# Kernel optimization log

Hardware: AMD Instinct MI355X
Metric: run time of the kernel (lower is better)

## Reference

```python
import jax, jax.numpy as jnp
import numpy as np

N, E, D, G, L = 100000, 1600000, 64, 512, 3
EPS = 1e-5


def setup_inputs() -> dict:
    key = jax.random.key(0)
    ks = jax.random.split(key, 8)
    x = jax.random.normal(ks[0], (N, D), dtype=jnp.float32)
    edge_index = jax.random.randint(ks[1], (2, E), 0, N, dtype=jnp.int32)
    batch = jnp.sort(jax.random.randint(ks[2], (N,), 0, G, dtype=jnp.int32))
    s = 1.0 / np.sqrt(D)
    convW = jax.random.normal(ks[3], (L, D, D), dtype=jnp.float32) * s
    convB = jnp.zeros((L, D), jnp.float32)
    bn_g = jnp.ones((L, D), jnp.float32); bn_b = jnp.zeros((L, D), jnp.float32)
    ln_g = jnp.ones((L, D), jnp.float32); ln_b = jnp.zeros((L, D), jnp.float32)
    W1 = jax.random.normal(ks[4], (3 * D, 2 * D), dtype=jnp.float32) * (1.0 / np.sqrt(3 * D))
    b1 = jnp.zeros((2 * D,), jnp.float32)
    ln1_g = jnp.ones((2 * D,), jnp.float32); ln1_b = jnp.zeros((2 * D,), jnp.float32)
    W2 = jax.random.normal(ks[5], (2 * D, D), dtype=jnp.float32) * (1.0 / np.sqrt(2 * D))
    b2 = jnp.zeros((D,), jnp.float32)
    ln2_g = jnp.ones((D,), jnp.float32); ln2_b = jnp.zeros((D,), jnp.float32)
    W3 = jax.random.normal(ks[6], (D, 1), dtype=jnp.float32) * s
    b3 = jnp.zeros((1,), jnp.float32)
    return dict(x=x, edge_index=edge_index, batch=batch, convW=convW, convB=convB,
                bn_g=bn_g, bn_b=bn_b, ln_g=ln_g, ln_b=ln_b,
                W1=W1, b1=b1, ln1_g=ln1_g, ln1_b=ln1_b,
                W2=W2, b2=b2, ln2_g=ln2_g, ln2_b=ln2_b, W3=W3, b3=b3)


def _layer_norm(h, g, b):
    mu = jnp.mean(h, axis=-1, keepdims=True)
    var = jnp.mean((h - mu) ** 2, axis=-1, keepdims=True)
    return (h - mu) * jax.lax.rsqrt(var + EPS) * g + b


def _forward(x, edge_index, batch, convW, convB, bn_g, bn_b, ln_g, ln_b,
             W1, b1, ln1_g, ln1_b, W2, b2, ln2_g, ln2_b, W3, b3):
    n = x.shape[0]
    loops = jnp.arange(n, dtype=edge_index.dtype)
    src = jnp.concatenate([edge_index[0], loops])  # self-loops as in GCNConv
    dst = jnp.concatenate([edge_index[1], loops])
    deg = jax.ops.segment_sum(jnp.ones_like(src, dtype=x.dtype), dst, num_segments=n)
    dinv = jnp.where(deg > 0, jax.lax.rsqrt(deg), 0.0)
    norm = (dinv[src] * dinv[dst])[:, None]  # [E+N, 1]

    h = x
    for i in range(L):
        x_in = h
        hw = h @ convW[i]                                   # [N, D]
        agg = jax.ops.segment_sum(norm * hw[src], dst, num_segments=n) + convB[i]
        # BatchNorm1d (train-mode batch stats, biased var)
        mu = jnp.mean(agg, axis=0)
        var = jnp.mean((agg - mu) ** 2, axis=0)
        hb = (agg - mu) * jax.lax.rsqrt(var + EPS) * bn_g[i] + bn_b[i]
        if i > 0:
            hb = hb + x_in  # residual (shapes match: D == D)
        h = jax.nn.gelu(_layer_norm(hb, ln_g[i], ln_b[i]), approximate=False)

    # multi-pool over graphs
    cnt = jax.ops.segment_sum(jnp.ones((n,), x.dtype), batch, num_segments=G)[:, None]
    s = jax.ops.segment_sum(h, batch, num_segments=G)
    mean = s / jnp.maximum(cnt, 1.0)
    mx = jax.ops.segment_max(h, batch, num_segments=G)
    mx = jnp.where(cnt > 0, mx, 0.0)
    z = jnp.concatenate([mean, mx, s], axis=1)  # [G, 3D]

    z = jax.nn.gelu(_layer_norm(z @ W1 + b1, ln1_g, ln1_b), approximate=False)
    z = jax.nn.gelu(_layer_norm(z @ W2 + b2, ln2_g, ln2_b), approximate=False)
    return z @ W3 + b3  # [G, num_classes]


def reference(x, edge_index, batch, convW, convB, bn_g, bn_b, ln_g, ln_b,
              W1, b1, ln1_g, ln1_b, W2, b2, ln2_g, ln2_b, W3, b3):
    return _forward(x, edge_index, batch, convW, convB, bn_g, bn_b, ln_g, ln_b,
                    W1, b1, ln1_g, ln1_b, W2, b2, ln2_g, ln2_b, W3, b3)
```

## Files before the change

kernel.cpp:

```cpp
#include <hip/hip_runtime.h>
#include <hip/hip_bf16.h>
#include <hip/hip_fp16.h>

#define DD 64
#define EPSV 1e-5f
#define NSLICE 16

typedef __attribute__((ext_vector_type(4))) _Float16 f16x4;
typedef __attribute__((ext_vector_type(8))) _Float16 f16x8;
typedef __attribute__((ext_vector_type(4))) float f32x4;

static __device__ __forceinline__ float fatomic_add(float* p, float v) {
#if defined(__HIP_DEVICE_COMPILE__)
    return unsafeAtomicAdd(p, v);
#else
    return 0.f;
#endif
}

static __device__ __forceinline__ float gelu_exact(float x) {
    return 0.5f * x * (1.0f + erff(x * 0.70710678118654752f));
}

static __device__ __forceinline__ void acc_u4(float* a8, uint4 v) {
    const __half2* hp = reinterpret_cast<const __half2*>(&v);
#pragma unroll
    for (int p = 0; p < 4; ++p) {
        float2 f = __half22float2(hp[p]);
        a8[2 * p] += f.x;
        a8[2 * p + 1] += f.y;
    }
}

#define ACHUNK 2048
#define NBMAX 400

__global__ __launch_bounds__(1024) void k_bcount(const int* __restrict__ dst,
                                                 int* __restrict__ bucketCnt,
                                                 int e, int nbuck) {
    __shared__ int h[NBMAX];
    int t = threadIdx.x;
    for (int i = t; i < nbuck; i += 1024) h[i] = 0;
    __syncthreads();
    int base = blockIdx.x * 8192;
#pragma unroll
    for (int k = 0; k < 8; ++k) {
        int i = base + k * 1024 + t;
        if (i < e) atomicAdd(&h[dst[i] >> 8], 1);
    }
    __syncthreads();
    for (int i = t; i < nbuck; i += 1024)
        if (h[i]) atomicAdd(&bucketCnt[i], h[i]);
}

__global__ __launch_bounds__(512) void k_bscan2(const int* __restrict__ bucketCnt,
                                                int* __restrict__ bbase,
                                                int* __restrict__ bcur,
                                                int* __restrict__ offs,
                                                int nbuck, int etotal, int n) {
    __shared__ int ws[8];
    int t = threadIdx.x, lane = t & 63, wv = t >> 6;
    int v = (t < nbuck) ? bucketCnt[t] : 0;
    int x = v;
#pragma unroll
    for (int o = 1; o < 64; o <<= 1) {
        int u = __shfl_up(x, o, 64);
        if (lane >= o) x += u;
    }
    if (lane == 63) ws[wv] = x;
    __syncthreads();
    int add = 0;
    for (int w = 0; w < wv; ++w) add += ws[w];
    int excl = add + x - v;
    if (t < nbuck) {
        bbase[t] = excl;
        bcur[t] = excl;
    }
    if (t == 0) {
        bbase[nbuck] = etotal;
        offs[n] = etotal;
    }
}

__global__ __launch_bounds__(1024) void k_dhist(const int* __restrict__ off,
                                                int* __restrict__ dcount,
                                                const int* __restrict__ batch,
                                                int* __restrict__ bnd,
                                                __half* __restrict__ mA,
                                                __half* __restrict__ mB,
                                                int n, int g) {
    __shared__ int h[256];
    int t = threadIdx.x;
    if (t < 256) h[t] = 0;
    __syncthreads();
    int i = blockIdx.x * 1024 + t;
    if (i < n) {
        int d = min(off[i + 1] - off[i], 255);
        atomicAdd(&h[d], 1);
        int b = batch[i];
        if (i == 0)
            for (int q = 0; q <= b; ++q) bnd[q] = 0;
        else {
            int pb = batch[i - 1];
            for (int q = pb + 1; q <= b; ++q) bnd[q] = i;
        }
        if (i == n - 1)
            for (int q = b + 1; q <= g; ++q) bnd[q] = n;
    }
    if (blockIdx.x == 0 && t < 64) {
        mA[(size_t)n * 64 + t] = __float2half_rn(0.f);
        mB[(size_t)n * 64 + t] = __float2half_rn(0.f);
    }
    __syncthreads();
    if (t < 256 && h[t]) atomicAdd(&dcount[t], h[t]);
}

__global__ __launch_bounds__(256) void k_dscan(const int* __restrict__ dcount,
                                               int* __restrict__ dcur) {
    __shared__ int ws[4];
    int t = threadIdx.x;
    int lane = t & 63, wv = t >> 6;
    int v = dcount[t];
    int x = v;
#pragma unroll
    for (int o = 1; o < 64; o <<= 1) {
        int u = __shfl_up(x, o, 64);
        if (lane >= o) x += u;
    }
    if (lane == 63) ws[wv] = x;
    __syncthreads();
    int add = 0;
    for (int w = 0; w < wv; ++w) add += ws[w];
    dcur[t] = add + x - v;
}

__global__ __launch_bounds__(1024) void k_dscatter(const int* __restrict__ off,
                                                   int* __restrict__ dcur,
                                                   int* __restrict__ perm, int n) {
    __shared__ int lcnt[256], lbase[256];
    int t = threadIdx.x;
    if (t < 256) lcnt[t] = 0;
    __syncthreads();
    int i = blockIdx.x * 1024 + t;
    int d = 0, rank = 0;
    if (i < n) {
        d = min(off[i + 1] - off[i], 255);
        rank = atomicAdd(&lcnt[d], 1);
    }
    __syncthreads();
    if (t < 256 && lcnt[t]) lbase[t] = atomicAdd(&dcur[t], lcnt[t]);
    __syncthreads();
    if (i < n) perm[lbase[d] + rank] = i;
}

__global__ __launch_bounds__(1024) void k_slotinfo(const int* __restrict__ off,
                                                   const float* __restrict__ dinv,
                                                   const int* __restrict__ perm,
                                                   int4* __restrict__ sinfo,
                                                   int n, int ntiles) {
    int s = blockIdx.x * 1024 + threadIdx.x;
    if (s < n) {
        int node = perm[s];
        int a = off[node];
        int d = off[node + 1] - a;
        sinfo[s] = make_int4(a, d, node, __float_as_int(dinv[node]));
    } else if (s < ntiles * 16) {
        sinfo[s] = make_int4(0, 0, -1, 0);
    }
}

__global__ __launch_bounds__(256) void k_binA(const int* __restrict__ src,
                                              const int* __restrict__ dst,
                                              int* __restrict__ ebuf,
                                              int* __restrict__ bcur,
                                              int e, int nbuck) {
    __shared__ int cnt[NBMAX], startb[NBMAX], posb[NBMAX], gbase[NBMAX];
    __shared__ int stage[ACHUNK];
    __shared__ unsigned short stb[ACHUNK];
    int t = threadIdx.x;
    for (int cbase = blockIdx.x * ACHUNK; cbase < e; cbase += gridDim.x * ACHUNK) {
        int cval = min(ACHUNK, e - cbase);
        for (int i = t; i < nbuck; i += 256) { cnt[i] = 0; posb[i] = 0; }
        __syncthreads();
        int eb[8], es[8];
#pragma unroll
        for (int k = 0; k < 8; ++k) {
            int i = t + k * 256;
            if (i < cval) {
                int s = src[cbase + i];
                int d = dst[cbase + i];
                eb[k] = d >> 8;
                es[k] = s | ((d & 255) << 24);
                atomicAdd(&cnt[eb[k]], 1);
            } else eb[k] = -1;
        }
        __syncthreads();
        if (t == 0) {
            int r = 0;
            for (int b2 = 0; b2 < nbuck; ++b2) { startb[b2] = r; r += cnt[b2]; }
        }
        __syncthreads();
        for (int i = t; i < nbuck; i += 256)
            if (cnt[i] > 0) gbase[i] = atomicAdd(&bcur[i], cnt[i]);
#pragma unroll
        for (int k = 0; k < 8; ++k)
            if (eb[k] >= 0) {
                int idx = startb[eb[k]] + atomicAdd(&posb[eb[k]], 1);
                stage[idx] = es[k];
                stb[idx] = (unsigned short)eb[k];
            }
        __syncthreads();
        for (int i = t; i < cval; i += 256) {
            int b2 = stb[i];
            ebuf[gbase[b2] + (i - startb[b2])] = stage[i];
        }
        __syncthreads();
    }
}

__global__ __launch_bounds__(256) void k_binB(const int* __restrict__ ebuf,
                                              const int* __restrict__ bbase,
                                              const float* __restrict__ x,
                                              int* __restrict__ offs,
                                              float* __restrict__ dinv,
                                              __half* __restrict__ mA,
                                              int* __restrict__ csr, int n) {
    __shared__ int cnt[256], cur[256], ws[4];
    __shared__ float sdinv[256];
    int b = blockIdx.x;
    int base = b << 8;
    int nn = min(256, n - base);
    int t = threadIdx.x;
    int e0 = bbase[b], e1 = bbase[b + 1];
    cnt[t] = 0;
    __syncthreads();
    for (int i = e0 + t; i < e1; i += 256)
        atomicAdd(&cnt[((unsigned)ebuf[i]) >> 24], 1);
    __syncthreads();
    int v = cnt[t];
    int lane = t & 63, wv = t >> 6;
    int x2 = v;
#pragma unroll
    for (int o = 1; o < 64; o <<= 1) {
        int u = __shfl_up(x2, o, 64);
        if (lane >= o) x2 += u;
    }
    if (lane == 63) ws[wv] = x2;
    __syncthreads();
    int add = 0;
    for (int w = 0; w < wv; ++w) add += ws[w];
    int excl = add + x2 - v;
    float dv = rsqrtf((float)v + 1.0f);
    if (t < nn) {
        offs[base + t] = e0 + excl;
        dinv[base + t] = dv;
    }
    sdinv[t] = dv;
    cur[t] = e0 + excl;
    __syncthreads();
    const int tot = nn * 64;
    const size_t gbase2 = (size_t)base * 64;
    for (int i = t; i < tot; i += 256) {
        float val = x[gbase2 + i] * sdinv[i >> 6];
        mA[gbase2 + i] = __float2half_rn(val);
    }
    for (int i = e0 + t; i < e1; i += 256) {
        int packed = ebuf[i];
        int dl = ((unsigned)packed) >> 24;
        int pos = atomicAdd(&cur[dl], 1);
        csr[pos] = packed & 0x00FFFFFF;
    }
}

__global__ __launch_bounds__(256, 4) void k_gather_gemm(const int4* __restrict__ sinfo,
                                                        const int* __restrict__ csr,
                                                        const __half* __restrict__ m16,
                                                        const float* __restrict__ W,
                                                        const float* __restrict__ convB,
                                                        __half* __restrict__ agg,
                                                        float* __restrict__ gstat,
                                                        int n, int nzero) {
    __shared__ float sred[128];
    const int t = threadIdx.x;
    const int lane = t & 63, wv = t >> 6;
    const int g = lane >> 4, ln = lane & 15;

    f16x8 bfr[2][4];
#pragma unroll
    for (int kt = 0; kt < 2; ++kt)
#pragma unroll
        for (int nt = 0; nt < 4; ++nt) {
            f16x8 h;
#pragma unroll
            for (int j = 0; j < 8; ++j)
                h[j] = (_Float16)W[(32 * kt + 8 * g + j) * 64 + 16 * nt + ln];
            bfr[kt][nt] = h;
        }
    const float bias[4] = {convB[ln], convB[16 + ln], convB[32 + ln], convB[48 + ln]};

    if (t < 128) sred[t] = 0.f;
    __syncthreads();

    const int ntiles = (n + 15) >> 4;
    const int tile = blockIdx.x * 4 + wv;
    float s_acc[4] = {0.f, 0.f, 0.f, 0.f}, q_acc[4] = {0.f, 0.f, 0.f, 0.f};
    const uint4* mrow4 = (const uint4*)m16;

    if (tile < ntiles) {
        const int4 si = sinfo[tile * 16 + ln];
        const int a = si.x, deg = si.y, node = si.z;
        const float dd = __int_as_float(si.w);
        const int row_self = (node >= 0) ? node : nzero;

        int md = deg;
#pragma unroll
        for (int o = 1; o < 64; o <<= 1) md = max(md, __shfl_xor(md, o, 64));

        float acc[2][8];
#pragma unroll
        for (int kt = 0; kt < 2; ++kt)
#pragma unroll
            for (int j = 0; j < 8; ++j) acc[kt][j] = 0.f;

        {
            const uint4* rp = mrow4 + ((size_t)row_self << 3) + g;
            uint4 v0 = rp[0], v1 = rp[4];
            acc_u4(acc[0], v0);
            acc_u4(acc[1], v1);
        }
        int ecur[4];
#pragma unroll
        for (int k = 0; k < 4; ++k) ecur[k] = (k < deg) ? csr[a + k] : nzero;
        for (int i = 0; i < md; i += 4) {
            int enx[4];
#pragma unroll
            for (int k = 0; k < 4; ++k) enx[k] = (i + 4 + k < deg) ? csr[a + i + 4 + k] : nzero;
            uint4 v[4][2];
#pragma unroll
            for (int r = 0; r < 4; ++r) {
                const uint4* rp = mrow4 + ((size_t)ecur[r] << 3) + g;
                v[r][0] = rp[0];
                v[r][1] = rp[4];
            }
#pragma unroll
            for (int r = 0; r < 4; ++r) {
                acc_u4(acc[0], v[r][0]);
                acc_u4(acc[1], v[r][1]);
            }
#pragma unroll
            for (int k = 0; k < 4; ++k) ecur[k] = enx[k];
        }

        f32x4 c[4];
#pragma unroll
        for (int nt = 0; nt < 4; ++nt) c[nt] = (f32x4){0.f, 0.f, 0.f, 0.f};
#pragma unroll
        for (int kt = 0; kt < 2; ++kt) {
            f16x8 ah, ar;
#pragma unroll
            for (int j = 0; j < 8; ++j) {
                float v = acc[kt][j] * dd;
                _Float16 h = (_Float16)v;
                ah[j] = h;
                ar[j] = (_Float16)(v - (float)h);
            }
#pragma unroll
            for (int nt = 0; nt < 4; ++nt) {
                c[nt] = __builtin_amdgcn_mfma_f32_16x16x32_f16(ah, bfr[kt][nt], c[nt], 0, 0, 0);
                c[nt] = __builtin_amdgcn_mfma_f32_16x16x32_f16(ar, bfr[kt][nt], c[nt], 0, 0, 0);
            }
        }

        int prow[4];
#pragma unroll
        for (int i = 0; i < 4; ++i) prow[i] = __shfl(node, 4 * g + i, 64);
#pragma unroll
        for (int nt = 0; nt < 4; ++nt) {
#pragma unroll
            for (int i = 0; i < 4; ++i) {
                if (prow[i] >= 0) {
                    float v = c[nt][i] + bias[nt];
                    agg[(size_t)prow[i] * 64 + 16 * nt + ln] = __float2half_rn(v);
                    s_acc[nt] += v;
                    q_acc[nt] += v * v;
                }
            }
        }
    }

#pragma unroll
    for (int nt = 0; nt < 4; ++nt) {
        s_acc[nt] += __shfl_xor(s_acc[nt], 16, 64);
        s_acc[nt] += __shfl_xor(s_acc[nt], 32, 64);
        q_acc[nt] += __shfl_xor(q_acc[nt], 16, 64);
        q_acc[nt] += __shfl_xor(q_acc[nt], 32, 64);
    }
    if (g == 0) {
#pragma unroll
        for (int nt = 0; nt < 4; ++nt) {
            atomicAdd(&sred[16 * nt + ln], s_acc[nt]);
            atomicAdd(&sred[64 + 16 * nt + ln], q_acc[nt]);
        }
    }
    __syncthreads();
    if (t < 64) {
        float* gs = gstat + (blockIdx.x & (NSLICE - 1)) * 128;
        fatomic_add(&gs[t], sred[t]);
        fatomic_add(&gs[64 + t], sred[64 + t]);
    }
}

__global__ __launch_bounds__(256) void k_bn_ln_gelu(const __half* __restrict__ agg,
                                                    const __half* __restrict__ m16res,
                                                    const float* __restrict__ gstat,
                                                    const float* __restrict__ dinv,
                                                    const float* __restrict__ bng,
                                                    const float* __restrict__ bnb,
                                                    const float* __restrict__ lng,
                                                    const float* __restrict__ lnb,
                                                    __half* __restrict__ m16out,
                                                    int n, int has_res, int scale_out) {
    int t = threadIdx.x;
    int lane = t & 63, wv = t >> 6;
    float fs = 0.f, fq = 0.f;
#pragma unroll
    for (int s = 0; s < NSLICE; ++s) {
        fs += gstat[s * 128 + lane];
        fq += gstat[s * 128 + 64 + lane];
    }
    float invN = 1.0f / (float)n;
    float mu_c = fs * invN;
    float var_c = fq * invN - mu_c * mu_c;
    float bscale = rsqrtf(var_c + EPSV) * bng[lane];
    float bshift = bnb[lane];
    float lg = lng[lane], lb = lnb[lane];
    for (int r = blockIdx.x * 4 + wv; r < n; r += gridDim.x * 4) {
        float dd = dinv[r];
        float x = __half2float(agg[(size_t)r * 64 + lane]);
        float hb = (x - mu_c) * bscale + bshift;
        if (has_res) hb += __half2float(m16res[(size_t)r * 64 + lane]) * (1.0f / dd);
        float ssum = hb;
#pragma unroll
        for (int off = 32; off; off >>= 1) ssum += __shfl_xor(ssum, off, 64);
        float rmu = ssum * (1.f / 64.f);
        float d = hb - rmu;
        float vs = d * d;
#pragma unroll
        for (int off = 32; off; off >>= 1) vs += __shfl_xor(vs, off, 64);
        float rvar = vs * (1.f / 64.f);
        float ln = d * rsqrtf(rvar + EPSV) * lg + lb;
        float g = gelu_exact(ln);
        float outv = scale_out ? g * dd : g;
        m16out[(size_t)r * 64 + lane] = __float2half_rn(outv);
    }
}

__global__ __launch_bounds__(256) void k_poolhead(const __half* __restrict__ h,
                                                  const int* __restrict__ bnd,
                                                  const float* __restrict__ W1, const float* __restrict__ b1,
                                                  const float* __restrict__ ln1g, const float* __restrict__ ln1b,
                                                  const float* __restrict__ W2, const float* __restrict__ b2,
                                                  const float* __restrict__ ln2g, const float* __restrict__ ln2b,
                                                  const float* __restrict__ W3, const float* __restrict__ b3,
                                                  float* __restrict__ out) {
    int g = blockIdx.x;
    int t = threadIdx.x;
    int lane = t & 63, wv = t >> 6;
    __shared__ float ss[256], sm[256], zl[192], h1[128], red[2];
    int s0 = bnd[g], e0 = bnd[g + 1];
    float s = 0.f, mx = -INFINITY;
    for (int i = s0 + wv; i < e0; i += 4) {
        float v = __half2float(h[(size_t)i * 64 + lane]);
        s += v;
        mx = fmaxf(mx, v);
    }
    ss[t] = s;
    sm[t] = mx;
    __syncthreads();
    if (t < 64) {
        float fs = ss[t] + ss[t + 64] + ss[t + 128] + ss[t + 192];
        float fm = fmaxf(fmaxf(sm[t], sm[t + 64]), fmaxf(sm[t + 128], sm[t + 192]));
        float cntf = (float)(e0 - s0);
        float mean = fs / fmaxf(cntf, 1.0f);
        if (e0 == s0) fm = 0.f;
        zl[t] = mean;
        zl[64 + t] = fm;
        zl[128 + t] = fs;
    }
    __syncthreads();
    float acc = 0.f;
    if (t < 128) {
        acc = b1[t];
        for (int k = 0; k < 192; ++k) acc += zl[k] * W1[k * 128 + t];
    }
    float s1 = acc;
#pragma unroll
    for (int off = 32; off; off >>= 1) s1 += __shfl_xor(s1, off, 64);
    if (lane == 0 && wv < 2) red[wv] = s1;
    __syncthreads();
    float mu = (red[0] + red[1]) * (1.f / 128.f);
    float d = acc - mu;
    float q = d * d;
#pragma unroll
    for (int off = 32; off; off >>= 1) q += __shfl_xor(q, off, 64);
    __syncthreads();
    if (lane == 0 && wv < 2) red[wv] = q;
    __syncthreads();
    float var = (red[0] + red[1]) * (1.f / 128.f);
    if (t < 128) {
        float ln = d * rsqrtf(var + EPSV) * ln1g[t] + ln1b[t];
        h1[t] = gelu_exact(ln);
    }
    __syncthreads();
    if (t < 64) {
        float acc2 = b2[t];
        for (int k = 0; k < 128; ++k) acc2 += h1[k] * W2[k * 64 + t];
        float s2 = acc2;
#pragma unroll
        for (int off = 32; off; off >>= 1) s2 += __shfl_xor(s2, off, 64);
        float mu2 = s2 * (1.f / 64.f);
        float d2 = acc2 - mu2;
        float q2 = d2 * d2;
#pragma unroll
        for (int off = 32; off; off >>= 1) q2 += __shfl_xor(q2, off, 64);
        float var2 = q2 * (1.f / 64.f);
        float l2 = d2 * rsqrtf(var2 + EPSV) * ln2g[t] + ln2b[t];
        float g2 = gelu_exact(l2);
        float p = g2 * W3[t];
#pragma unroll
        for (int off = 32; off; off >>= 1) p += __shfl_xor(p, off, 64);
        if (t == 0) out[g] = p + b3[0];
    }
}

extern "C" void kernel_launch(void* const* d_in, const int* in_sizes, int n_in,
                              void* d_out, int out_size, void* d_ws, size_t ws_size,
                              hipStream_t stream) {
    const float* x      = (const float*)d_in[0];
    const int*   eidx   = (const int*)d_in[1];
    const int*   batch  = (const int*)d_in[2];
    const float* convW  = (const float*)d_in[3];
    const float* convB  = (const float*)d_in[4];
    const float* bn_g   = (const float*)d_in[5];
    const float* bn_b   = (const float*)d_in[6];
    const float* ln_g   = (const float*)d_in[7];
    const float* ln_b   = (const float*)d_in[8];
    const float* W1     = (const float*)d_in[9];
    const float* b1     = (const float*)d_in[10];
    const float* ln1g   = (const float*)d_in[11];
    const float* ln1b   = (const float*)d_in[12];
    const float* W2     = (const float*)d_in[13];
    const float* b2     = (const float*)d_in[14];
    const float* ln2g   = (const float*)d_in[15];
    const float* ln2b   = (const float*)d_in[16];
    const float* W3     = (const float*)d_in[17];
    const float* b3     = (const float*)d_in[18];
    float* out = (float*)d_out;

    const int N = in_sizes[0] / DD;
    const int E = in_sizes[1] / 2;
    const int G = out_size;
    const int* esrc = eidx;
    const int* edst = eidx + E;

    char* ws = (char*)d_ws;
    size_t off_b = 0;
    auto alloc = [&](size_t bytes) {
        size_t p = off_b;
        off_b = (off_b + bytes + 255) & ~(size_t)255;
        return (void*)(ws + p);
    };
    const int ntiles = (N + 15) / 16;
    const int gblocks = (ntiles + 3) / 4;

    float*  gstats = (float*)alloc((size_t)3 * NSLICE * 128 * 4);
    int*    dcount = (int*)alloc(256 * 4);
    int*    bucketCnt = (int*)alloc((size_t)NBMAX * 4);
    const size_t zero_bytes = 3 * NSLICE * 128 * 4 + 1024 + 1792;
    int*    offs   = (int*)alloc((size_t)(N + 1) * 4);
    float*  dinv   = (float*)alloc((size_t)N * 4);
    int*    csr    = (int*)alloc((size_t)E * 4);
    int*    ebuf   = (int*)alloc((size_t)E * 4);
    __half* m16A   = (__half*)alloc((size_t)(N + 1) * DD * 2);
    __half* m16B   = (__half*)alloc((size_t)(N + 1) * DD * 2);
    __half* aggbuf = (__half*)alloc((size_t)N * DD * 2);
    int*    perm   = (int*)alloc((size_t)N * 4);
    int4*   sinfo  = (int4*)alloc((size_t)ntiles * 16 * 16);
    int*    dcur   = (int*)alloc(256 * 4);
    int*    bnd    = (int*)alloc((size_t)(G + 1) * 4);
    int*    bbase  = (int*)alloc((size_t)(NBMAX + 1) * 4);
    int*    bcur   = (int*)alloc(((size_t)(N + 255) / 256) * 4);
    (void)ws_size; (void)n_in;

    const int nbuck = (N + 255) / 256;
    const int nb = (N + 1023) / 1024;

    hipMemsetAsync(gstats, 0, zero_bytes, stream);
    k_bcount<<<(E + 8191) / 8192, 1024, 0, stream>>>(edst, bucketCnt, E, nbuck);
    k_bscan2<<<1, 512, 0, stream>>>(bucketCnt, bbase, bcur, offs, nbuck, E, N);
    k_binA<<<(E + ACHUNK - 1) / ACHUNK, 256, 0, stream>>>(esrc, edst, ebuf, bcur, E, nbuck);
    k_binB<<<nbuck, 256, 0, stream>>>(ebuf, bbase, x, offs, dinv, m16A, csr, N);
    k_dhist<<<nb, 1024, 0, stream>>>(offs, dcount, batch, bnd, m16A, m16B, N, G);
    k_dscan<<<1, 256, 0, stream>>>(dcount, dcur);
    k_dscatter<<<nb, 1024, 0, stream>>>(offs, dcur, perm, N);
    k_slotinfo<<<(ntiles * 16 + 1023) / 1024, 1024, 0, stream>>>(offs, dinv, perm, sinfo, N, ntiles);

    __half* gin[3]  = {m16A, m16B, m16A};
    __half* gout[3] = {m16B, m16A, m16B};

    for (int l = 0; l < 3; ++l) {
        float* gstat = gstats + (size_t)l * NSLICE * 128;
        k_gather_gemm<<<gblocks, 256, 0, stream>>>(sinfo, csr, (const __half*)gin[l],
                                                   convW + (size_t)l * DD * DD, convB + l * DD,
                                                   aggbuf, gstat, N, N);
        k_bn_ln_gelu<<<2048, 256, 0, stream>>>(aggbuf, gin[l], gstat, dinv,
                                               bn_g + l * DD, bn_b + l * DD,
                                               ln_g + l * DD, ln_b + l * DD,
                                               gout[l], N, l > 0 ? 1 : 0, l < 2 ? 1 : 0);
    }

    k_poolhead<<<G, 256, 0, stream>>>(m16B, bnd, W1, b1, ln1g, ln1b,
                                      W2, b2, ln2g, ln2b, W3, b3, out);
}
```

Baseline: 402.5 us.

## Fuse layer loop and pooling head into one cooperative persistent kernel

Replaces the per-layer gather-GEMM and BN/LN/GELU launches plus the pooling head with a single cooperative kernel of 1024 blocks. The blocks loop over tiles and rows and use grid.sync between phases, which removes seven kernel launches and their drain gaps. It also folds the slot-info construction into the degree scatter kernel, dropping the perm array and one launch. In exchange, the gather phase now runs with fewer resident waves over persistent loops, which may cut latency hiding, and grid-wide barriers add their own cost. The old multi-kernel path remains as a fallback if the cooperative launch fails.

```diff
diff --git a/kernel.cpp b/kernel.cpp
--- a/kernel.cpp
+++ b/kernel.cpp
@@ -1,12 +1,15 @@
 #include <hip/hip_runtime.h>
+#include <hip/hip_cooperative_groups.h>
 #include <hip/hip_bf16.h>
 #include <hip/hip_fp16.h>
+
+namespace cg = cooperative_groups;
 
 #define DD 64
 #define EPSV 1e-5f
 #define NSLICE 16
-
-typedef __attribute__((ext_vector_type(4))) _Float16 f16x4;
+#define CGBLOCKS 1024
+
 typedef __attribute__((ext_vector_type(8))) _Float16 f16x8;
 typedef __attribute__((ext_vector_type(4))) float f32x4;
 
@@ -88,7 +91,8 @@
                                                 int* __restrict__ bnd,
                                                 __half* __restrict__ mA,
                                                 __half* __restrict__ mB,
-                                                int n, int g) {
+                                                int4* __restrict__ sinfo,
+                                                int n, int g, int ntiles) {
     __shared__ int h[256];
     int t = threadIdx.x;
     if (t < 256) h[t] = 0;
@@ -111,6 +115,8 @@
         mA[(size_t)n * 64 + t] = __float2half_rn(0.f);
         mB[(size_t)n * 64 + t] = __float2half_rn(0.f);
     }
+    int pad = ntiles * 16 - n;
+    if (blockIdx.x == 0 && t < pad) sinfo[n + t] = make_int4(0, 0, -1, 0);
     __syncthreads();
     if (t < 256 && h[t]) atomicAdd(&dcount[t], h[t]);
 }
@@ -135,37 +141,27 @@
 }
 
 __global__ __launch_bounds__(1024) void k_dscatter(const int* __restrict__ off,
+                                                   const float* __restrict__ dinv,
                                                    int* __restrict__ dcur,
-                                                   int* __restrict__ perm, int n) {
+                                                   int4* __restrict__ sinfo, int n) {
     __shared__ int lcnt[256], lbase[256];
     int t = threadIdx.x;
     if (t < 256) lcnt[t] = 0;
     __syncthreads();
     int i = blockIdx.x * 1024 + t;
-    int d = 0, rank = 0;
+    int d = 0, rank = 0, a = 0, dtrue = 0;
     if (i < n) {
-        d = min(off[i + 1] - off[i], 255);
+        a = off[i];
+        dtrue = off[i + 1] - a;
+        d = min(dtrue, 255);
         rank = atomicAdd(&lcnt[d], 1);
     }
     __syncthreads();
     if (t < 256 && lcnt[t]) lbase[t] = atomicAdd(&dcur[t], lcnt[t]);
     __syncthreads();
-    if (i < n) perm[lbase[d] + rank] = i;
-}
-
-__global__ __launch_bounds__(1024) void k_slotinfo(const int* __restrict__ off,
-                                                   const float* __restrict__ dinv,
-                                                   const int* __restrict__ perm,
-                                                   int4* __restrict__ sinfo,
-                                                   int n, int ntiles) {
-    int s = blockIdx.x * 1024 + threadIdx.x;
-    if (s < n) {
-        int node = perm[s];
-        int a = off[node];
-        int d = off[node + 1] - a;
-        sinfo[s] = make_int4(a, d, node, __float_as_int(dinv[node]));
-    } else if (s < ntiles * 16) {
-        sinfo[s] = make_int4(0, 0, -1, 0);
+    if (i < n) {
+        int slot = lbase[d] + rank;
+        sinfo[slot] = make_int4(a, dtrue, i, __float_as_int(dinv[i]));
     }
 }
 
@@ -272,6 +268,284 @@
     }
 }
 
+static __device__ __forceinline__ void gather_tile(
+    const int4* __restrict__ sinfo, const int* __restrict__ csr,
+    const uint4* __restrict__ mrow4, const f16x8 bfr[2][4], const float bias[4],
+    __half* __restrict__ agg, int tile, int n, int lane, int g, int ln,
+    float s_acc[4], float q_acc[4]) {
+    const int4 si = sinfo[tile * 16 + ln];
+    const int a = si.x, deg = si.y, node = si.z;
+    const float dd = __int_as_float(si.w);
+    const int row_self = (node >= 0) ? node : n;
+
+    int md = deg;
+#pragma unroll
+    for (int o = 1; o < 64; o <<= 1) md = max(md, __shfl_xor(md, o, 64));
+
+    float acc[2][8];
+#pragma unroll
+    for (int kt = 0; kt < 2; ++kt)
+#pragma unroll
+        for (int j = 0; j < 8; ++j) acc[kt][j] = 0.f;
+
+    {
+        const uint4* rp = mrow4 + ((size_t)row_self << 3) + g;
+        uint4 v0 = rp[0], v1 = rp[4];
+        acc_u4(acc[0], v0);
+        acc_u4(acc[1], v1);
+    }
+    int ecur[4];
+#pragma unroll
+    for (int k = 0; k < 4; ++k) ecur[k] = (k < deg) ? csr[a + k] : n;
+    for (int i = 0; i < md; i += 4) {
+        int enx[4];
+#pragma unroll
+        for (int k = 0; k < 4; ++k) enx[k] = (i + 4 + k < deg) ? csr[a + i + 4 + k] : n;
+        uint4 v[4][2];
+#pragma unroll
+        for (int r = 0; r < 4; ++r) {
+            const uint4* rp = mrow4 + ((size_t)ecur[r] << 3) + g;
+            v[r][0] = rp[0];
+            v[r][1] = rp[4];
+        }
+#pragma unroll
+        for (int r = 0; r < 4; ++r) {
+            acc_u4(acc[0], v[r][0]);
+            acc_u4(acc[1], v[r][1]);
+        }
+#pragma unroll
+        for (int k = 0; k < 4; ++k) ecur[k] = enx[k];
+    }
+
+    f32x4 c[4];
+#pragma unroll
+    for (int nt = 0; nt < 4; ++nt) c[nt] = (f32x4){0.f, 0.f, 0.f, 0.f};
+#pragma unroll
+    for (int kt = 0; kt < 2; ++kt) {
+        f16x8 ah, ar;
+#pragma unroll
+        for (int j = 0; j < 8; ++j) {
+            float v = acc[kt][j] * dd;
+            _Float16 h = (_Float16)v;
+            ah[j] = h;
+            ar[j] = (_Float16)(v - (float)h);
+        }
+#pragma unroll
+        for (int nt = 0; nt < 4; ++nt) {
+            c[nt] = __builtin_amdgcn_mfma_f32_16x16x32_f16(ah, bfr[kt][nt], c[nt], 0, 0, 0);
+            c[nt] = __builtin_amdgcn_mfma_f32_16x16x32_f16(ar, bfr[kt][nt], c[nt], 0, 0, 0);
+        }
+    }
+
+    int prow[4];
+#pragma unroll
+    for (int i = 0; i < 4; ++i) prow[i] = __shfl(node, 4 * g + i, 64);
+#pragma unroll
+    for (int nt = 0; nt < 4; ++nt) {
+#pragma unroll
+        for (int i = 0; i < 4; ++i) {
+            if (prow[i] >= 0) {
+                float v = c[nt][i] + bias[nt];
+                agg[(size_t)prow[i] * 64 + 16 * nt + ln] = __float2half_rn(v);
+                s_acc[nt] += v;
+                q_acc[nt] += v * v;
+            }
+        }
+    }
+}
+
+static __device__ __forceinline__ void bn_row(
+    const __half* __restrict__ agg, const __half* __restrict__ res,
+    __half* __restrict__ gout, const float* __restrict__ dinv,
+    float mu_c, float bscale, float bshift, float lg, float lb,
+    int r, int lane, int has_res, int scale_out) {
+    float dd = dinv[r];
+    float xx = __half2float(agg[(size_t)r * 64 + lane]);
+    float hb = (xx - mu_c) * bscale + bshift;
+    if (has_res) hb += __half2float(res[(size_t)r * 64 + lane]) * (1.0f / dd);
+    float ssum = hb;
+#pragma unroll
+    for (int off = 32; off; off >>= 1) ssum += __shfl_xor(ssum, off, 64);
+    float rmu = ssum * (1.f / 64.f);
+    float d = hb - rmu;
+    float vs = d * d;
+#pragma unroll
+    for (int off = 32; off; off >>= 1) vs += __shfl_xor(vs, off, 64);
+    float rvar = vs * (1.f / 64.f);
+    float lnv = d * rsqrtf(rvar + EPSV) * lg + lb;
+    float gl = gelu_exact(lnv);
+    float outv = scale_out ? gl * dd : gl;
+    gout[(size_t)r * 64 + lane] = __float2half_rn(outv);
+}
+
+__global__ __launch_bounds__(256, 4) void k_layers(
+    const int4* __restrict__ sinfo, const int* __restrict__ csr,
+    const float* __restrict__ convW, const float* __restrict__ convB,
+    __half* __restrict__ m16A, __half* __restrict__ m16B,
+    __half* __restrict__ agg, float* __restrict__ gstats,
+    const float* __restrict__ dinv,
+    const float* __restrict__ bn_g, const float* __restrict__ bn_b,
+    const float* __restrict__ ln_g, const float* __restrict__ ln_b,
+    const int* __restrict__ bnd,
+    const float* __restrict__ W1, const float* __restrict__ b1,
+    const float* __restrict__ ln1g, const float* __restrict__ ln1b,
+    const float* __restrict__ W2, const float* __restrict__ b2,
+    const float* __restrict__ ln2g, const float* __restrict__ ln2b,
+    const float* __restrict__ W3, const float* __restrict__ b3,
+    float* __restrict__ out, int n, int G) {
+    cg::grid_group grid = cg::this_grid();
+    __shared__ float smem[896];
+    const int t = threadIdx.x;
+    const int lane = t & 63, wv = t >> 6;
+    const int g = lane >> 4, ln = lane & 15;
+    const int ntiles = (n + 15) >> 4;
+    const int NW = gridDim.x << 2;
+
+    for (int l = 0; l < 3; ++l) {
+        const __half* gin = (l == 1) ? m16B : m16A;
+        __half* gout = (l == 1) ? m16A : m16B;
+        const uint4* mrow4 = (const uint4*)gin;
+        const float* W = convW + (size_t)l * 4096;
+        float* gstat = gstats + (size_t)l * NSLICE * 128;
+
+        f16x8 bfr[2][4];
+#pragma unroll
+        for (int kt = 0; kt < 2; ++kt)
+#pragma unroll
+            for (int nt = 0; nt < 4; ++nt) {
+                f16x8 h;
+#pragma unroll
+                for (int j = 0; j < 8; ++j)
+                    h[j] = (_Float16)W[(32 * kt + 8 * g + j) * 64 + 16 * nt + ln];
+                bfr[kt][nt] = h;
+            }
+        const float bias[4] = {convB[l * 64 + ln], convB[l * 64 + 16 + ln],
+                               convB[l * 64 + 32 + ln], convB[l * 64 + 48 + ln]};
+        float* sred = smem;
+        if (t < 128) sred[t] = 0.f;
+        __syncthreads();
+
+        float s_acc[4] = {0.f, 0.f, 0.f, 0.f}, q_acc[4] = {0.f, 0.f, 0.f, 0.f};
+        for (int tile = blockIdx.x * 4 + wv; tile < ntiles; tile += NW)
+            gather_tile(sinfo, csr, mrow4, bfr, bias, agg, tile, n, lane, g, ln, s_acc, q_acc);
+#pragma unroll
+        for (int nt = 0; nt < 4; ++nt) {
+            s_acc[nt] += __shfl_xor(s_acc[nt], 16, 64);
+            s_acc[nt] += __shfl_xor(s_acc[nt], 32, 64);
+            q_acc[nt] += __shfl_xor(q_acc[nt], 16, 64);
+            q_acc[nt] += __shfl_xor(q_acc[nt], 32, 64);
+        }
+        if (g == 0) {
+#pragma unroll
+            for (int nt = 0; nt < 4; ++nt) {
+                atomicAdd(&sred[16 * nt + ln], s_acc[nt]);
+                atomicAdd(&sred[64 + 16 * nt + ln], q_acc[nt]);
+            }
+        }
+        __syncthreads();
+        if (t < 64) {
+            float* gs = gstat + (blockIdx.x & (NSLICE - 1)) * 128;
+            fatomic_add(&gs[t], sred[t]);
+            fatomic_add(&gs[64 + t], sred[64 + t]);
+        }
+        grid.sync();
+
+        {
+            float fs = 0.f, fq = 0.f;
+#pragma unroll
+            for (int s2 = 0; s2 < NSLICE; ++s2) {
+                fs += gstat[s2 * 128 + lane];
+                fq += gstat[s2 * 128 + 64 + lane];
+            }
+            float invN = 1.0f / (float)n;
+            float mu_c = fs * invN;
+            float var_c = fq * invN - mu_c * mu_c;
+            float bscale = rsqrtf(var_c + EPSV) * bn_g[l * 64 + lane];
+            float bshift = bn_b[l * 64 + lane];
+            float lg = ln_g[l * 64 + lane], lb = ln_b[l * 64 + lane];
+            const int has_res = (l > 0), scale_out = (l < 2);
+            for (int r = blockIdx.x * 4 + wv; r < n; r += NW)
+                bn_row(agg, gin, gout, dinv, mu_c, bscale, bshift, lg, lb, r, lane,
+                       has_res, scale_out);
+        }
+        grid.sync();
+    }
+
+    if (blockIdx.x < (unsigned)G) {
+        const __half* h = m16B;
+        int gph = blockIdx.x;
+        float* ss = smem;
+        float* sm = smem + 256;
+        float* zl = smem + 512;
+        float* h1 = smem + 704;
+        float* red = smem + 832;
+        int s0 = bnd[gph], e0 = bnd[gph + 1];
+        float s = 0.f, mx = -INFINITY;
+        for (int i = s0 + wv; i < e0; i += 4) {
+            float v = __half2float(h[(size_t)i * 64 + lane]);
+            s += v;
+            mx = fmaxf(mx, v);
+        }
+        ss[t] = s;
+        sm[t] = mx;
+        __syncthreads();
+        if (t < 64) {
+            float fs = ss[t] + ss[t + 64] + ss[t + 128] + ss[t + 192];
+            float fm = fmaxf(fmaxf(sm[t], sm[t + 64]), fmaxf(sm[t + 128], sm[t + 192]));
+            float cntf = (float)(e0 - s0);
+            float mean = fs / fmaxf(cntf, 1.0f);
+            if (e0 == s0) fm = 0.f;
+            zl[t] = mean;
+            zl[64 + t] = fm;
+            zl[128 + t] = fs;
+        }
+        __syncthreads();
+        float acc = 0.f;
+        if (t < 128) {
+            acc = b1[t];
+            for (int k = 0; k < 192; ++k) acc += zl[k] * W1[k * 128 + t];
+        }
+        float s1 = acc;
+#pragma unroll
+        for (int off = 32; off; off >>= 1) s1 += __shfl_xor(s1, off, 64);
+        if (lane == 0 && wv < 2) red[wv] = s1;
+        __syncthreads();
+        float mu = (red[0] + red[1]) * (1.f / 128.f);
+        float d = acc - mu;
+        float q = d * d;
+#pragma unroll
+        for (int off = 32; off; off >>= 1) q += __shfl_xor(q, off, 64);
+        __syncthreads();
+        if (lane == 0 && wv < 2) red[wv] = q;
+        __syncthreads();
+        float var = (red[0] + red[1]) * (1.f / 128.f);
+        if (t < 128) {
+            float lnv = d * rsqrtf(var + EPSV) * ln1g[t] + ln1b[t];
+            h1[t] = gelu_exact(lnv);
+        }
+        __syncthreads();
+        if (t < 64) {
+            float acc2 = b2[t];
+            for (int k = 0; k < 128; ++k) acc2 += h1[k] * W2[k * 64 + t];
+            float s2 = acc2;
+#pragma unroll
+            for (int off = 32; off; off >>= 1) s2 += __shfl_xor(s2, off, 64);
+            float mu2 = s2 * (1.f / 64.f);
+            float d2 = acc2 - mu2;
+            float q2 = d2 * d2;
+#pragma unroll
+            for (int off = 32; off; off >>= 1) q2 += __shfl_xor(q2, off, 64);
+            float var2 = q2 * (1.f / 64.f);
+            float l2 = d2 * rsqrtf(var2 + EPSV) * ln2g[t] + ln2b[t];
+            float g2 = gelu_exact(l2);
+            float p = g2 * W3[t];
+#pragma unroll
+            for (int off = 32; off; off >>= 1) p += __shfl_xor(p, off, 64);
+            if (t == 0) out[gph] = p + b3[0];
+        }
+    }
+}
+
 __global__ __launch_bounds__(256, 4) void k_gather_gemm(const int4* __restrict__ sinfo,
                                                         const int* __restrict__ csr,
                                                         const __half* __restrict__ m16,
@@ -279,12 +553,11 @@
                                                         const float* __restrict__ convB,
                                                         __half* __restrict__ agg,
                                                         float* __restrict__ gstat,
-                                                        int n, int nzero) {
+                                                        int n) {
     __shared__ float sred[128];
     const int t = threadIdx.x;
     const int lane = t & 63, wv = t >> 6;
     const int g = lane >> 4, ln = lane & 15;
-
     f16x8 bfr[2][4];
 #pragma unroll
     for (int kt = 0; kt < 2; ++kt)
@@ -297,97 +570,14 @@
             bfr[kt][nt] = h;
         }
     const float bias[4] = {convB[ln], convB[16 + ln], convB[32 + ln], convB[48 + ln]};
-
     if (t < 128) sred[t] = 0.f;
     __syncthreads();
-
     const int ntiles = (n + 15) >> 4;
     const int tile = blockIdx.x * 4 + wv;
     float s_acc[4] = {0.f, 0.f, 0.f, 0.f}, q_acc[4] = {0.f, 0.f, 0.f, 0.f};
-    const uint4* mrow4 = (const uint4*)m16;
-
-    if (tile < ntiles) {
-        const int4 si = sinfo[tile * 16 + ln];
-        const int a = si.x, deg = si.y, node = si.z;
-        const float dd = __int_as_float(si.w);
-        const int row_self = (node >= 0) ? node : nzero;
-
-        int md = deg;
-#pragma unroll
-        for (int o = 1; o < 64; o <<= 1) md = max(md, __shfl_xor(md, o, 64));
-
-        float acc[2][8];
-#pragma unroll
-        for (int kt = 0; kt < 2; ++kt)
-#pragma unroll
-            for (int j = 0; j < 8; ++j) acc[kt][j] = 0.f;
-
-        {
-            const uint4* rp = mrow4 + ((size_t)row_self << 3) + g;
-            uint4 v0 = rp[0], v1 = rp[4];
-            acc_u4(acc[0], v0);
-            acc_u4(acc[1], v1);
-        }
-        int ecur[4];
-#pragma unroll
-        for (int k = 0; k < 4; ++k) ecur[k] = (k < deg) ? csr[a + k] : nzero;
-        for (int i = 0; i < md; i += 4) {
-            int enx[4];
-#pragma unroll
-            for (int k = 0; k < 4; ++k) enx[k] = (i + 4 + k < deg) ? csr[a + i + 4 + k] : nzero;
-            uint4 v[4][2];
-#pragma unroll
-            for (int r = 0; r < 4; ++r) {
-                const uint4* rp = mrow4 + ((size_t)ecur[r] << 3) + g;
-                v[r][0] = rp[0];
-                v[r][1] = rp[4];
-            }
-#pragma unroll
-            for (int r = 0; r < 4; ++r) {
-                acc_u4(acc[0], v[r][0]);
-                acc_u4(acc[1], v[r][1]);
-            }
-#pragma unroll
-            for (int k = 0; k < 4; ++k) ecur[k] = enx[k];
-        }
-
-        f32x4 c[4];
-#pragma unroll
-        for (int nt = 0; nt < 4; ++nt) c[nt] = (f32x4){0.f, 0.f, 0.f, 0.f};
-#pragma unroll
-        for (int kt = 0; kt < 2; ++kt) {
-            f16x8 ah, ar;
-#pragma unroll
-            for (int j = 0; j < 8; ++j) {
-                float v = acc[kt][j] * dd;
-                _Float16 h = (_Float16)v;
-                ah[j] = h;
-                ar[j] = (_Float16)(v - (float)h);
-            }
-#pragma unroll
-            for (int nt = 0; nt < 4; ++nt) {
-                c[nt] = __builtin_amdgcn_mfma_f32_16x16x32_f16(ah, bfr[kt][nt], c[nt], 0, 0, 0);
-                c[nt] = __builtin_amdgcn_mfma_f32_16x16x32_f16(ar, bfr[kt][nt], c[nt], 0, 0, 0);
-            }
-        }
-
-        int prow[4];
-#pragma unroll
-        for (int i = 0; i < 4; ++i) prow[i] = __shfl(node, 4 * g + i, 64);
-#pragma unroll
-        for (int nt = 0; nt < 4; ++nt) {
-#pragma unroll
-            for (int i = 0; i < 4; ++i) {
-                if (prow[i] >= 0) {
-                    float v = c[nt][i] + bias[nt];
-                    agg[(size_t)prow[i] * 64 + 16 * nt + ln] = __float2half_rn(v);
-                    s_acc[nt] += v;
-                    q_acc[nt] += v * v;
-                }
-            }
-        }
-    }
-
+    if (tile < ntiles)
+        gather_tile(sinfo, csr, (const uint4*)m16, bfr, bias, agg, tile, n, lane, g, ln,
+                    s_acc, q_acc);
 #pragma unroll
     for (int nt = 0; nt < 4; ++nt) {
         s_acc[nt] += __shfl_xor(s_acc[nt], 16, 64);
@@ -434,25 +624,9 @@
     float bscale = rsqrtf(var_c + EPSV) * bng[lane];
     float bshift = bnb[lane];
     float lg = lng[lane], lb = lnb[lane];
-    for (int r = blockIdx.x * 4 + wv; r < n; r += gridDim.x * 4) {
-        float dd = dinv[r];
-        float x = __half2float(agg[(size_t)r * 64 + lane]);
-        float hb = (x - mu_c) * bscale + bshift;
-        if (has_res) hb += __half2float(m16res[(size_t)r * 64 + lane]) * (1.0f / dd);
-        float ssum = hb;
-#pragma unroll
-        for (int off = 32; off; off >>= 1) ssum += __shfl_xor(ssum, off, 64);
-        float rmu = ssum * (1.f / 64.f);
-        float d = hb - rmu;
-        float vs = d * d;
-#pragma unroll
-        for (int off = 32; off; off >>= 1) vs += __shfl_xor(vs, off, 64);
-        float rvar = vs * (1.f / 64.f);
-        float ln = d * rsqrtf(rvar + EPSV) * lg + lb;
-        float g = gelu_exact(ln);
-        float outv = scale_out ? g * dd : g;
-        m16out[(size_t)r * 64 + lane] = __float2half_rn(outv);
-    }
+    for (int r = blockIdx.x * 4 + wv; r < n; r += gridDim.x * 4)
+        bn_row(agg, m16res, m16out, dinv, mu_c, bscale, bshift, lg, lb, r, lane,
+               has_res, scale_out);
 }
 
 __global__ __launch_bounds__(256) void k_poolhead(const __half* __restrict__ h,
@@ -508,8 +682,8 @@
     __syncthreads();
     float var = (red[0] + red[1]) * (1.f / 128.f);
     if (t < 128) {
-        float ln = d * rsqrtf(var + EPSV) * ln1g[t] + ln1b[t];
-        h1[t] = gelu_exact(ln);
+        float lnv = d * rsqrtf(var + EPSV) * ln1g[t] + ln1b[t];
+        h1[t] = gelu_exact(lnv);
     }
     __syncthreads();
     if (t < 64) {
@@ -571,7 +745,6 @@
         return (void*)(ws + p);
     };
     const int ntiles = (N + 15) / 16;
-    const int gblocks = (ntiles + 3) / 4;
 
     float*  gstats = (float*)alloc((size_t)3 * NSLICE * 128 * 4);
     int*    dcount = (int*)alloc(256 * 4);
@@ -584,7 +757,6 @@
     __half* m16A   = (__half*)alloc((size_t)(N + 1) * DD * 2);
     __half* m16B   = (__half*)alloc((size_t)(N + 1) * DD * 2);
     __half* aggbuf = (__half*)alloc((size_t)N * DD * 2);
-    int*    perm   = (int*)alloc((size_t)N * 4);
     int4*   sinfo  = (int4*)alloc((size_t)ntiles * 16 * 16);
     int*    dcur   = (int*)alloc(256 * 4);
     int*    bnd    = (int*)alloc((size_t)(G + 1) * 4);
@@ -600,25 +772,35 @@
     k_bscan2<<<1, 512, 0, stream>>>(bucketCnt, bbase, bcur, offs, nbuck, E, N);
     k_binA<<<(E + ACHUNK - 1) / ACHUNK, 256, 0, stream>>>(esrc, edst, ebuf, bcur, E, nbuck);
     k_binB<<<nbuck, 256, 0, stream>>>(ebuf, bbase, x, offs, dinv, m16A, csr, N);
-    k_dhist<<<nb, 1024, 0, stream>>>(offs, dcount, batch, bnd, m16A, m16B, N, G);
+    k_dhist<<<nb, 1024, 0, stream>>>(offs, dcount, batch, bnd, m16A, m16B, sinfo, N, G, ntiles);
     k_dscan<<<1, 256, 0, stream>>>(dcount, dcur);
-    k_dscatter<<<nb, 1024, 0, stream>>>(offs, dcur, perm, N);
-    k_slotinfo<<<(ntiles * 16 + 1023) / 1024, 1024, 0, stream>>>(offs, dinv, perm, sinfo, N, ntiles);
-
-    __half* gin[3]  = {m16A, m16B, m16A};
-    __half* gout[3] = {m16B, m16A, m16B};
-
-    for (int l = 0; l < 3; ++l) {
-        float* gstat = gstats + (size_t)l * NSLICE * 128;
-        k_gather_gemm<<<gblocks, 256, 0, stream>>>(sinfo, csr, (const __half*)gin[l],
-                                                   convW + (size_t)l * DD * DD, convB + l * DD,
-                                                   aggbuf, gstat, N, N);
-        k_bn_ln_gelu<<<2048, 256, 0, stream>>>(aggbuf, gin[l], gstat, dinv,
-                                               bn_g + l * DD, bn_b + l * DD,
-                                               ln_g + l * DD, ln_b + l * DD,
-                                               gout[l], N, l > 0 ? 1 : 0, l < 2 ? 1 : 0);
-    }
-
-    k_poolhead<<<G, 256, 0, stream>>>(m16B, bnd, W1, b1, ln1g, ln1b,
-                                      W2, b2, ln2g, ln2b, W3, b3, out);
-}
+    k_dscatter<<<nb, 1024, 0, stream>>>(offs, dinv, dcur, sinfo, N);
+
+    int Nv = N, Gv = G;
+    void* args[] = {
+        (void*)&sinfo, (void*)&csr, (void*)&convW, (void*)&convB,
+        (void*)&m16A, (void*)&m16B, (void*)&aggbuf, (void*)&gstats,
+        (void*)&dinv, (void*)&bn_g, (void*)&bn_b, (void*)&ln_g, (void*)&ln_b,
+        (void*)&bnd, (void*)&W1, (void*)&b1, (void*)&ln1g, (void*)&ln1b,
+        (void*)&W2, (void*)&b2, (void*)&ln2g, (void*)&ln2b,
+        (void*)&W3, (void*)&b3, (void*)&out, (void*)&Nv, (void*)&Gv};
+    hipError_t cerr = hipLaunchCooperativeKernel((void*)k_layers, dim3(CGBLOCKS),
+                                                 dim3(256), args, 0, stream);
+    if (cerr != hipSuccess) {
+        const int gblocks = (ntiles + 3) / 4;
+        __half* gin[3]  = {m16A, m16B, m16A};
+        __half* gout[3] = {m16B, m16A, m16B};
+        for (int l = 0; l < 3; ++l) {
+            float* gstat = gstats + (size_t)l * NSLICE * 128;
+            k_gather_gemm<<<gblocks, 256, 0, stream>>>(sinfo, csr, (const __half*)gin[l],
+                                                       convW + (size_t)l * DD * DD,
+                                                       convB + l * DD, aggbuf, gstat, N);
+            k_bn_ln_gelu<<<2048, 256, 0, stream>>>(aggbuf, gin[l], gstat, dinv,
+                                                   bn_g + l * DD, bn_b + l * DD,
+                                                   ln_g + l * DD, ln_b + l * DD,
+                                                   gout[l], N, l > 0 ? 1 : 0, l < 2 ? 1 : 0);
+        }
+        k_poolhead<<<G, 256, 0, stream>>>(m16B, bnd, W1, b1, ln1g, ln1b,
+                                          W2, b2, ln2g, ln2b, W3, b3, out);
+    }
+}
```

After: 1.160 ms. 188% more time.
